# Kernel tuning notes

Hardware: AMD Instinct MI355X
Metric: run time of the kernel (lower is better)

## Reference

```python
import jax, jax.numpy as jnp
import numpy as np

N = 100000   # total nodes
E = 1600000  # total edges
B = 256      # graphs per batch
F_NODE, F_EDGE, H = 35, 10, 64
N_CONV = 3
IN_DIM = 2 * H + F_EDGE  # 138
EPS = 1e-5


def setup_inputs() -> dict:
    key = jax.random.key(0)
    ks = jax.random.split(key, 16)
    node_features = jax.random.normal(ks[0], (N, F_NODE), dtype=jnp.float32)
    edge_index = jax.random.randint(ks[1], (2, E), 0, N, dtype=jnp.int64)
    edge_features = jax.random.uniform(ks[2], (E, F_EDGE), dtype=jnp.float32)
    graph_index = jnp.sort(jax.random.randint(ks[3], (N,), 0, B, dtype=jnp.int64))
    s = lambda fan_in: 1.0 / np.sqrt(fan_in)
    embed_w = jax.random.uniform(ks[4], (F_NODE, H), jnp.float32, -s(F_NODE), s(F_NODE))
    embed_b = jax.random.uniform(ks[5], (H,), jnp.float32, -s(F_NODE), s(F_NODE))
    gate_w = jax.random.uniform(ks[6], (N_CONV, IN_DIM, H), jnp.float32, -s(IN_DIM), s(IN_DIM))
    gate_b = jax.random.uniform(ks[7], (N_CONV, H), jnp.float32, -s(IN_DIM), s(IN_DIM))
    cand_w = jax.random.uniform(ks[8], (N_CONV, IN_DIM, H), jnp.float32, -s(IN_DIM), s(IN_DIM))
    cand_b = jax.random.uniform(ks[9], (N_CONV, H), jnp.float32, -s(IN_DIM), s(IN_DIM))
    bn_g = jnp.ones((N_CONV, H), dtype=jnp.float32)
    bn_b = jnp.zeros((N_CONV, H), dtype=jnp.float32)
    mlp_w1 = jax.random.uniform(ks[10], (H, 128), jnp.float32, -s(H), s(H))
    mlp_b1 = jax.random.uniform(ks[11], (128,), jnp.float32, -s(H), s(H))
    mlp_w2 = jax.random.uniform(ks[12], (128, 64), jnp.float32, -s(128), s(128))
    mlp_b2 = jax.random.uniform(ks[13], (64,), jnp.float32, -s(128), s(128))
    mlp_w3 = jax.random.uniform(ks[14], (64, 1), jnp.float32, -s(64), s(64))
    mlp_b3 = jax.random.uniform(ks[15], (1,), jnp.float32, -s(64), s(64))
    return dict(node_features=node_features, edge_index=edge_index,
                edge_features=edge_features, graph_index=graph_index,
                embed_w=embed_w, embed_b=embed_b,
                gate_w=gate_w, gate_b=gate_b, cand_w=cand_w, cand_b=cand_b,
                bn_g=bn_g, bn_b=bn_b,
                mlp_w1=mlp_w1, mlp_b1=mlp_b1, mlp_w2=mlp_w2, mlp_b2=mlp_b2,
                mlp_w3=mlp_w3, mlp_b3=mlp_b3)


def _conv(h, src, dst, edge_feat, gw, gb, cw, cb, gamma, beta):
    # gather -> concat -> gated message
    z = jnp.concatenate([h[src], h[dst], edge_feat], axis=1)  # [E, 2H+F_edge]
    g = jax.nn.sigmoid(z @ gw + gb)
    c = jax.nn.softplus(z @ cw + cb)
    m = g * c
    # scatter-add onto source nodes
    agg = jax.ops.segment_sum(m, src, num_segments=h.shape[0])
    # BatchNorm1d (training-mode batch stats, biased variance)
    mu = agg.mean(axis=0)
    var = agg.var(axis=0)
    agg_bn = (agg - mu) * jax.lax.rsqrt(var + EPS) * gamma + beta
    return jax.nn.softplus(h + agg_bn)


def reference(node_features, edge_index, edge_features, graph_index,
              embed_w, embed_b, gate_w, gate_b, cand_w, cand_b, bn_g, bn_b,
              mlp_w1, mlp_b1, mlp_w2, mlp_b2, mlp_w3, mlp_b3):
    src, dst = edge_index[0], edge_index[1]
    h = node_features @ embed_w + embed_b  # [N, H]
    for i in range(N_CONV):
        h = _conv(h, src, dst, edge_features,
                  gate_w[i], gate_b[i], cand_w[i], cand_b[i], bn_g[i], bn_b[i])
    # mean pool per graph (B is static = 256)
    pooled = jax.ops.segment_sum(h, graph_index, num_segments=B)
    counts = jax.ops.segment_sum(jnp.ones((h.shape[0],), h.dtype), graph_index, num_segments=B)
    pooled = pooled / jnp.clip(counts, 1.0, None)[:, None]
    x = jax.nn.softplus(pooled @ mlp_w1 + mlp_b1)
    x = jax.nn.softplus(x @ mlp_w2 + mlp_b2)
    return (x @ mlp_w3 + mlp_b3)[:, 0]  # [B]
```

## Files before the change

kernel.cpp:

```cpp
#include <hip/hip_runtime.h>
#include <hip/hip_bf16.h>

#define NN 100000
#define EE 1600000
#define BB 256
#define F_NODE 35
#define F_EDGE 10
#define HH 64
#define IN_DIM 138
#define N_CONV 3
#define EPSBN 1e-5f
#define NB1 ((NN + 255) / 256)

#define NWAVES 2000
#define NGROUPS 50
#define SUBLEN 200
#define EPW 800
#define EFSTR 12

typedef _Float16 half8 __attribute__((ext_vector_type(8)));
typedef float floatx4 __attribute__((ext_vector_type(4)));

__device__ __forceinline__ float softplus_fast(float x) {
    return fmaxf(x, 0.0f) + __logf(1.0f + __expf(-fabsf(x)));
}
__device__ __forceinline__ float sigmoid_fast(float x) {
    return __builtin_amdgcn_rcpf(1.0f + __expf(-x));
}

__global__ __launch_bounds__(256)
void hist_kernel(const int* __restrict__ src, int* __restrict__ cnt) {
    int e = blockIdx.x * 256 + threadIdx.x;
    atomicAdd(&cnt[src[e]], 1);
}

__global__ __launch_bounds__(256)
void scan1_kernel(int* __restrict__ cnt, int* __restrict__ bsum, int n) {
    __shared__ int ls[256];
    int t = threadIdx.x;
    int i = blockIdx.x * 256 + t;
    int v = (i < n) ? cnt[i] : 0;
    ls[t] = v;
    __syncthreads();
#pragma unroll
    for (int off = 1; off < 256; off <<= 1) {
        int add = (t >= off) ? ls[t - off] : 0;
        __syncthreads();
        ls[t] += add;
        __syncthreads();
    }
    if (i < n) cnt[i] = ls[t] - v;
    if (t == 255) bsum[blockIdx.x] = ls[255];
}

__global__ __launch_bounds__(512)
void scan2_kernel(int* __restrict__ bsum, int nb) {
    __shared__ int ls[512];
    int t = threadIdx.x;
    int v = (t < nb) ? bsum[t] : 0;
    ls[t] = v;
    __syncthreads();
#pragma unroll
    for (int off = 1; off < 512; off <<= 1) {
        int add = (t >= off) ? ls[t - off] : 0;
        __syncthreads();
        ls[t] += add;
        __syncthreads();
    }
    if (t < nb) bsum[t] = ls[t] - v;
}

__global__ __launch_bounds__(256)
void scan3_kernel(int* __restrict__ cnt, const int* __restrict__ bsum, int n) {
    int i = blockIdx.x * 256 + threadIdx.x;
    if (i < n) cnt[i] += bsum[blockIdx.x];
}

__global__ __launch_bounds__(256)
void scatter_kernel(const int* __restrict__ src, const int* __restrict__ dst,
                    const float* __restrict__ ef,
                    int* __restrict__ offs,
                    int* __restrict__ ssorted, int* __restrict__ dsorted,
                    _Float16* __restrict__ ef16) {
    int e = blockIdx.x * 256 + threadIdx.x;
    int s = src[e];
    int pos = atomicAdd(&offs[s], 1);
    ssorted[pos] = s;
    dsorted[pos] = dst[e];
    const float* efe = ef + (size_t)e * F_EDGE;
    uint* op = (uint*)(ef16 + (size_t)pos * EFSTR);
#pragma unroll
    for (int i = 0; i < 5; i++) {
        _Float16 h0 = (_Float16)efe[2 * i];
        _Float16 h1 = (_Float16)efe[2 * i + 1];
        op[i] = (uint)*(unsigned short*)&h0 | ((uint)*(unsigned short*)&h1 << 16);
    }
    op[5] = 0u;
}

__global__ __launch_bounds__(256)
void prep_w_kernel(const float* __restrict__ gw, const float* __restrict__ cw,
                   _Float16* __restrict__ wT) {
    int idx = blockIdx.x * 256 + threadIdx.x;
    if (idx >= 3 * 128 * 160) return;
    int k = idx % 160;
    int n = (idx / 160) & 127;
    int layer = idx / (160 * 128);
    float v = 0.f;
    if (k < IN_DIM)
        v = (n < 64) ? gw[layer * IN_DIM * HH + k * HH + n]
                     : cw[layer * IN_DIM * HH + k * HH + (n - 64)];
    wT[idx] = (_Float16)v;
}

__global__ __launch_bounds__(256)
void embed_kernel(const float* __restrict__ nf, const float* __restrict__ w,
                  const float* __restrict__ bias, float* __restrict__ h,
                  _Float16* __restrict__ h16, int n) {
    __shared__ float wl[F_NODE * HH];
    int tid = threadIdx.x;
    for (int i = tid; i < F_NODE * HH; i += 256) wl[i] = w[i];
    __syncthreads();
    int idx = blockIdx.x * 256 + tid;
    int node = idx >> 6, j = idx & 63;
    if (node >= n) return;
    float acc = bias[j];
    const float* row = nf + node * F_NODE;
#pragma unroll
    for (int k = 0; k < F_NODE; k++) acc += row[k] * wl[k * HH + j];
    h[idx] = acc;
    h16[idx] = (_Float16)acc;
}

__device__ __forceinline__ void load_A(const _Float16* __restrict__ h16,
                                       const _Float16* __restrict__ ef16,
                                       int s, int d, int eg, int quad,
                                       uint4& A0, uint4& A1, uint4& A2, uint4& A3,
                                       uint4& A4) {
    const uint4* hs = (const uint4*)(h16 + (size_t)s * HH);
    const uint4* hd = (const uint4*)(h16 + (size_t)d * HH);
    A0 = hs[quad];
    A1 = hs[quad + 4];
    A2 = hd[quad];
    A3 = hd[quad + 4];
    uint4 z; z.x = z.y = z.z = z.w = 0u;
    A4 = z;
    const _Float16* p = ef16 + (size_t)eg * EFSTR;
    if (quad == 0) {
        uint2 a = *(const uint2*)p;
        uint2 b = *(const uint2*)(p + 4);
        A4.x = a.x; A4.y = a.y; A4.z = b.x; A4.w = b.y;
    } else if (quad == 1) {
        uint2 a = *(const uint2*)(p + 8);
        A4.x = a.x; A4.y = a.y;
    }
}

__global__ __launch_bounds__(64, 2)
void edge_conv_mfma(const _Float16* __restrict__ h16,
                    const int* __restrict__ esrc,
                    const int* __restrict__ edst,
                    const _Float16* __restrict__ ef16,
                    const _Float16* __restrict__ wT,
                    const float* __restrict__ gb, const float* __restrict__ cb,
                    float* __restrict__ agg) {
    int lane = threadIdx.x;
    int quad = lane >> 4, n15 = lane & 15;
    int base = blockIdx.x * EPW + ((n15 >> 2) * SUBLEN) + (n15 & 3);

    half8 B[8][5];
#pragma unroll
    for (int t = 0; t < 8; t++) {
        const _Float16* wr = wT + (t * 16 + n15) * 160 + quad * 8;
#pragma unroll
        for (int ks = 0; ks < 5; ks++)
            B[t][ks] = *(const half8*)(wr + ks * 32);
    }
    float gb0 = gb[n15], gb1 = gb[16 + n15], gb2 = gb[32 + n15], gb3 = gb[48 + n15];
    float cb0 = cb[n15], cb1 = cb[16 + n15], cb2 = cb[32 + n15], cb3 = cb[48 + n15];

    int sprev = -1;
    float am0 = 0.f, am1 = 0.f, am2 = 0.f, am3 = 0.f;

    int eg = base;
    int s = esrc[eg], d = edst[eg];
    uint4 A0, A1, A2, A3, A4;
    load_A(h16, ef16, s, d, eg, quad, A0, A1, A2, A3, A4);
    int egn = base + 4;
    int sn = esrc[egn], dn = edst[egn];

    for (int g = 0; g < NGROUPS; g++) {
        int s_cur = s;

        floatx4 acc[8];
#pragma unroll
        for (int t = 0; t < 8; t++) acc[t] = (floatx4){0.f, 0.f, 0.f, 0.f};

        half8 a0 = __builtin_bit_cast(half8, A0);
        half8 a1 = __builtin_bit_cast(half8, A1);
        half8 a2 = __builtin_bit_cast(half8, A2);
        half8 a3 = __builtin_bit_cast(half8, A3);
        half8 a4 = __builtin_bit_cast(half8, A4);
#pragma unroll
        for (int t = 0; t < 8; t++) acc[t] = __builtin_amdgcn_mfma_f32_16x16x32_f16(a0, B[t][0], acc[t], 0, 0, 0);
#pragma unroll
        for (int t = 0; t < 8; t++) acc[t] = __builtin_amdgcn_mfma_f32_16x16x32_f16(a1, B[t][1], acc[t], 0, 0, 0);
#pragma unroll
        for (int t = 0; t < 8; t++) acc[t] = __builtin_amdgcn_mfma_f32_16x16x32_f16(a2, B[t][2], acc[t], 0, 0, 0);
#pragma unroll
        for (int t = 0; t < 8; t++) acc[t] = __builtin_amdgcn_mfma_f32_16x16x32_f16(a3, B[t][3], acc[t], 0, 0, 0);
#pragma unroll
        for (int t = 0; t < 8; t++) acc[t] = __builtin_amdgcn_mfma_f32_16x16x32_f16(a4, B[t][4], acc[t], 0, 0, 0);

        int egc = base + ((g + 1 < NGROUPS) ? (g + 1) * 4 : g * 4);
        load_A(h16, ef16, sn, dn, egc, quad, A0, A1, A2, A3, A4);
        s = sn; d = dn;
        int eg2 = base + ((g + 2 < NGROUPS) ? (g + 2) * 4 : (NGROUPS - 1) * 4);
        sn = esrc[eg2]; dn = edst[eg2];

#pragma unroll
        for (int r = 0; r < 4; r++) {
            int sr = __shfl(s_cur, quad * 4 + r, 64);
            if (sr != sprev) {
                if (sprev >= 0) {
                    float* p = agg + (size_t)sprev * HH + n15;
                    atomicAdd(p, am0);
                    atomicAdd(p + 16, am1);
                    atomicAdd(p + 32, am2);
                    atomicAdd(p + 48, am3);
                }
                sprev = sr;
                am0 = am1 = am2 = am3 = 0.f;
            }
            am0 += sigmoid_fast(acc[0][r] + gb0) * softplus_fast(acc[4][r] + cb0);
            am1 += sigmoid_fast(acc[1][r] + gb1) * softplus_fast(acc[5][r] + cb1);
            am2 += sigmoid_fast(acc[2][r] + gb2) * softplus_fast(acc[6][r] + cb2);
            am3 += sigmoid_fast(acc[3][r] + gb3) * softplus_fast(acc[7][r] + cb3);
        }
    }
    if (sprev >= 0) {
        float* p = agg + (size_t)sprev * HH + n15;
        atomicAdd(p, am0);
        atomicAdd(p + 16, am1);
        atomicAdd(p + 32, am2);
        atomicAdd(p + 48, am3);
    }
}

__global__ __launch_bounds__(256)
void bn_stats_kernel(const float* __restrict__ agg, float* __restrict__ stats, int total) {
    __shared__ float ls[256], lss[256];
    int tid = threadIdx.x;
    float s = 0.f, ss = 0.f;
    for (int idx = blockIdx.x * 256 + tid; idx < total; idx += gridDim.x * 256) {
        float v = agg[idx];
        s += v;
        ss += v * v;
    }
    ls[tid] = s;
    lss[tid] = ss;
    __syncthreads();
    if (tid < 64) {
        s = ls[tid] + ls[tid + 64] + ls[tid + 128] + ls[tid + 192];
        ss = lss[tid] + lss[tid + 64] + lss[tid + 128] + lss[tid + 192];
        atomicAdd(&stats[tid], s);
        atomicAdd(&stats[64 + tid], ss);
    }
}

__global__ __launch_bounds__(256)
void bn_update_kernel(float* __restrict__ h, _Float16* __restrict__ h16,
                      const float* __restrict__ agg,
                      const float* __restrict__ stats,
                      const float* __restrict__ g, const float* __restrict__ b,
                      int total, float invN) {
    int idx = blockIdx.x * 256 + threadIdx.x;
    if (idx >= total) return;
    int j = idx & 63;
    float mu = stats[j] * invN;
    float var = stats[64 + j] * invN - mu * mu;
    var = fmaxf(var, 0.0f);
    float scale = g[j] * rsqrtf(var + EPSBN);
    float v = h[idx] + (agg[idx] - mu) * scale + b[j];
    float hv = softplus_fast(v);
    h[idx] = hv;
    h16[idx] = (_Float16)hv;
}

__global__ __launch_bounds__(256)
void pool_kernel(const float* __restrict__ h, const int* __restrict__ gi,
                 float* __restrict__ pool, float* __restrict__ counts, int n) {
    int tid = threadIdx.x;
    int grp = tid >> 6;
    int j = tid & 63;
    int n0 = blockIdx.x * 64 + grp * 16;
    if (n0 >= n) return;
    int nend = n0 + 16; if (nend > n) nend = n;
    int gprev = gi[n0];
    float a = 0.f;
    int cnt = 0;
    for (int nn = n0; nn < nend; nn++) {
        int gg = gi[nn];
        if (gg != gprev) {
            atomicAdd(&pool[gprev * 64 + j], a);
            if (j == 0) atomicAdd(&counts[gprev], (float)cnt);
            a = 0.f; cnt = 0; gprev = gg;
        }
        a += h[(size_t)nn * 64 + j];
        cnt++;
    }
    atomicAdd(&pool[gprev * 64 + j], a);
    if (j == 0) atomicAdd(&counts[gprev], (float)cnt);
}

__global__ __launch_bounds__(128)
void mlp_kernel(const float* __restrict__ pool, const float* __restrict__ counts,
                const float* __restrict__ w1, const float* __restrict__ b1,
                const float* __restrict__ w2, const float* __restrict__ b2,
                const float* __restrict__ w3, const float* __restrict__ b3,
                float* __restrict__ out) {
    __shared__ float x0[64], x1[128], x2[64];
    int b = blockIdx.x, t = threadIdx.x;
    if (t < 64) {
        float c = counts[b];
        c = c < 1.f ? 1.f : c;
        x0[t] = pool[b * 64 + t] / c;
    }
    __syncthreads();
    {
        float acc = 0.f;
#pragma unroll
        for (int k = 0; k < 64; k++) acc += x0[k] * w1[k * 128 + t];
        x1[t] = softplus_fast(acc + b1[t]);
    }
    __syncthreads();
    if (t < 64) {
        float acc = 0.f;
#pragma unroll
        for (int k = 0; k < 128; k++) acc += x1[k] * w2[k * 64 + t];
        x2[t] = softplus_fast(acc + b2[t]);
    }
    __syncthreads();
    if (t == 0) {
        float acc = 0.f;
        for (int k = 0; k < 64; k++) acc += x2[k] * w3[k];
        out[b] = acc + b3[0];
    }
}

extern "C" void kernel_launch(void* const* d_in, const int* in_sizes, int n_in,
                              void* d_out, int out_size, void* d_ws, size_t ws_size,
                              hipStream_t stream) {
    const float* nf      = (const float*)d_in[0];
    const int*   ei      = (const int*)d_in[1];
    const float* ef      = (const float*)d_in[2];
    const int*   gi      = (const int*)d_in[3];
    const float* embed_w = (const float*)d_in[4];
    const float* embed_b = (const float*)d_in[5];
    const float* gate_w  = (const float*)d_in[6];
    const float* gate_b  = (const float*)d_in[7];
    const float* cand_w  = (const float*)d_in[8];
    const float* cand_b  = (const float*)d_in[9];
    const float* bn_g    = (const float*)d_in[10];
    const float* bn_b    = (const float*)d_in[11];
    const float* w1      = (const float*)d_in[12];
    const float* b1      = (const float*)d_in[13];
    const float* w2      = (const float*)d_in[14];
    const float* b2      = (const float*)d_in[15];
    const float* w3      = (const float*)d_in[16];
    const float* b3      = (const float*)d_in[17];
    float* out = (float*)d_out;

    const int NH = NN * HH;
    char* p = (char*)d_ws;
    float*     h       = (float*)p;            p += (size_t)NH * 4;
    float*     agg     = (float*)p;            p += (size_t)NH * 4;
    float*     stats   = (float*)p;            p += 128 * 4;
    _Float16*  h16     = (_Float16*)p;         p += (size_t)NH * 2;
    int*       ssorted = (int*)p;              p += (size_t)EE * 4;
    int*       dsorted = (int*)p;              p += (size_t)EE * 4;
    _Float16*  ef16    = (_Float16*)p;         p += (size_t)EE * EFSTR * 2;
    _Float16*  wTall   = (_Float16*)p;         p += (size_t)3 * 128 * 160 * 2;
    int*       offs    = (int*)p;              p += (size_t)NN * 4;
    int*       bsum    = (int*)p;              p += 512 * 4;
    float*     pool    = (float*)p;            p += (size_t)BB * HH * 4;
    float*     counts  = (float*)p;            p += (size_t)BB * 4;

    const int* src = ei;
    const int* dst = ei + EE;

    hipMemsetAsync(offs, 0, (size_t)NN * 4, stream);
    hist_kernel<<<EE / 256, 256, 0, stream>>>(src, offs);
    prep_w_kernel<<<(3 * 128 * 160 + 255) / 256, 256, 0, stream>>>(gate_w, cand_w, wTall);
    scan1_kernel<<<NB1, 256, 0, stream>>>(offs, bsum, NN);
    scan2_kernel<<<1, 512, 0, stream>>>(bsum, NB1);
    scan3_kernel<<<NB1, 256, 0, stream>>>(offs, bsum, NN);
    scatter_kernel<<<EE / 256, 256, 0, stream>>>(src, dst, ef, offs, ssorted, dsorted, ef16);

    embed_kernel<<<NH / 256, 256, 0, stream>>>(nf, embed_w, embed_b, h, h16, NN);

    for (int i = 0; i < N_CONV; i++) {
        hipMemsetAsync(agg, 0, ((size_t)NH + 128) * 4, stream);
        edge_conv_mfma<<<NWAVES, 64, 0, stream>>>(
            h16, ssorted, dsorted, ef16,
            wTall + (size_t)i * 128 * 160,
            gate_b + i * HH, cand_b + i * HH, agg);
        bn_stats_kernel<<<512, 256, 0, stream>>>(agg, stats, NH);
        bn_update_kernel<<<NH / 256, 256, 0, stream>>>(
            h, h16, agg, stats, bn_g + i * HH, bn_b + i * HH, NH, 1.0f / (float)NN);
    }

    hipMemsetAsync(pool, 0, (size_t)(BB * HH + BB) * 4, stream);
    pool_kernel<<<(NN + 63) / 64, 256, 0, stream>>>(h, gi, pool, counts, NN);
    mlp_kernel<<<BB, 128, 0, stream>>>(pool, counts, w1, b1, w2, b2, w3, b3, out);
}
```

Before: 969.0 us.

## Build edge sort via rank/perm gather and fold agg zeroing into BN update

Records each edge's rank during the histogram atomics, then builds a permutation and gathers edge data in sorted order. This replaces the scatter kernel's second round of atomics and its scattered writes with coalesced writes and gathered reads, and reads edge features as float2. It also merges all memsets into one at the start, keeps per-layer stats buffers, and has bn_update zero agg after reading it, so the per-layer memsets go away. The cost is an extra kernel launch and two extra E-sized buffers (perm, rank).

New measurement: 895.0 us. -7.6%, faster.

```diff
diff --git a/kernel.cpp b/kernel.cpp
--- a/kernel.cpp
+++ b/kernel.cpp
@@ -29,9 +29,10 @@
 }
 
 __global__ __launch_bounds__(256)
-void hist_kernel(const int* __restrict__ src, int* __restrict__ cnt) {
+void hist_rank_kernel(const int* __restrict__ src, int* __restrict__ cnt,
+                      int* __restrict__ rank) {
     int e = blockIdx.x * 256 + threadIdx.x;
-    atomicAdd(&cnt[src[e]], 1);
+    rank[e] = atomicAdd(&cnt[src[e]], 1);
 }
 
 __global__ __launch_bounds__(256)
@@ -77,22 +78,29 @@
 }
 
 __global__ __launch_bounds__(256)
-void scatter_kernel(const int* __restrict__ src, const int* __restrict__ dst,
-                    const float* __restrict__ ef,
-                    int* __restrict__ offs,
-                    int* __restrict__ ssorted, int* __restrict__ dsorted,
-                    _Float16* __restrict__ ef16) {
+void perm_kernel(const int* __restrict__ src, const int* __restrict__ rank,
+                 const int* __restrict__ offs, int* __restrict__ perm) {
     int e = blockIdx.x * 256 + threadIdx.x;
-    int s = src[e];
-    int pos = atomicAdd(&offs[s], 1);
-    ssorted[pos] = s;
+    perm[offs[src[e]] + rank[e]] = e;
+}
+
+__global__ __launch_bounds__(256)
+void gather_kernel(const int* __restrict__ perm,
+                   const int* __restrict__ src, const int* __restrict__ dst,
+                   const float* __restrict__ ef,
+                   int* __restrict__ ssorted, int* __restrict__ dsorted,
+                   _Float16* __restrict__ ef16) {
+    int pos = blockIdx.x * 256 + threadIdx.x;
+    int e = perm[pos];
+    ssorted[pos] = src[e];
     dsorted[pos] = dst[e];
-    const float* efe = ef + (size_t)e * F_EDGE;
+    const float2* efe = (const float2*)(ef + (size_t)e * F_EDGE);
     uint* op = (uint*)(ef16 + (size_t)pos * EFSTR);
 #pragma unroll
     for (int i = 0; i < 5; i++) {
-        _Float16 h0 = (_Float16)efe[2 * i];
-        _Float16 h1 = (_Float16)efe[2 * i + 1];
+        float2 v = efe[i];
+        _Float16 h0 = (_Float16)v.x;
+        _Float16 h1 = (_Float16)v.y;
         op[i] = (uint)*(unsigned short*)&h0 | ((uint)*(unsigned short*)&h1 << 16);
     }
     op[5] = 0u;
@@ -270,7 +278,7 @@
 
 __global__ __launch_bounds__(256)
 void bn_update_kernel(float* __restrict__ h, _Float16* __restrict__ h16,
-                      const float* __restrict__ agg,
+                      float* __restrict__ agg,
                       const float* __restrict__ stats,
                       const float* __restrict__ g, const float* __restrict__ b,
                       int total, float invN) {
@@ -281,7 +289,9 @@
     float var = stats[64 + j] * invN - mu * mu;
     var = fmaxf(var, 0.0f);
     float scale = g[j] * rsqrtf(var + EPSBN);
-    float v = h[idx] + (agg[idx] - mu) * scale + b[j];
+    float a = agg[idx];
+    agg[idx] = 0.f;
+    float v = h[idx] + (a - mu) * scale + b[j];
     float hv = softplus_fast(v);
     h[idx] = hv;
     h16[idx] = (_Float16)hv;
@@ -373,44 +383,47 @@
 
     const int NH = NN * HH;
     char* p = (char*)d_ws;
+    int*       offs    = (int*)p;              p += (size_t)NN * 4;
+    float*     agg     = (float*)p;            p += (size_t)NH * 4;
+    float*     stats   = (float*)p;            p += 3 * 128 * 4;
+    float*     pool    = (float*)p;            p += (size_t)BB * HH * 4;
+    float*     counts  = (float*)p;            p += (size_t)BB * 4;
+    size_t zero_bytes = (size_t)(p - (char*)d_ws);
     float*     h       = (float*)p;            p += (size_t)NH * 4;
-    float*     agg     = (float*)p;            p += (size_t)NH * 4;
-    float*     stats   = (float*)p;            p += 128 * 4;
     _Float16*  h16     = (_Float16*)p;         p += (size_t)NH * 2;
     int*       ssorted = (int*)p;              p += (size_t)EE * 4;
     int*       dsorted = (int*)p;              p += (size_t)EE * 4;
     _Float16*  ef16    = (_Float16*)p;         p += (size_t)EE * EFSTR * 2;
+    int*       perm    = (int*)p;              p += (size_t)EE * 4;
+    int*       rank    = (int*)p;              p += (size_t)EE * 4;
     _Float16*  wTall   = (_Float16*)p;         p += (size_t)3 * 128 * 160 * 2;
-    int*       offs    = (int*)p;              p += (size_t)NN * 4;
     int*       bsum    = (int*)p;              p += 512 * 4;
-    float*     pool    = (float*)p;            p += (size_t)BB * HH * 4;
-    float*     counts  = (float*)p;            p += (size_t)BB * 4;
 
     const int* src = ei;
     const int* dst = ei + EE;
 
-    hipMemsetAsync(offs, 0, (size_t)NN * 4, stream);
-    hist_kernel<<<EE / 256, 256, 0, stream>>>(src, offs);
+    hipMemsetAsync(d_ws, 0, zero_bytes, stream);
+
+    hist_rank_kernel<<<EE / 256, 256, 0, stream>>>(src, offs, rank);
     prep_w_kernel<<<(3 * 128 * 160 + 255) / 256, 256, 0, stream>>>(gate_w, cand_w, wTall);
     scan1_kernel<<<NB1, 256, 0, stream>>>(offs, bsum, NN);
     scan2_kernel<<<1, 512, 0, stream>>>(bsum, NB1);
     scan3_kernel<<<NB1, 256, 0, stream>>>(offs, bsum, NN);
-    scatter_kernel<<<EE / 256, 256, 0, stream>>>(src, dst, ef, offs, ssorted, dsorted, ef16);
+    perm_kernel<<<EE / 256, 256, 0, stream>>>(src, rank, offs, perm);
+    gather_kernel<<<EE / 256, 256, 0, stream>>>(perm, src, dst, ef, ssorted, dsorted, ef16);
 
     embed_kernel<<<NH / 256, 256, 0, stream>>>(nf, embed_w, embed_b, h, h16, NN);
 
     for (int i = 0; i < N_CONV; i++) {
-        hipMemsetAsync(agg, 0, ((size_t)NH + 128) * 4, stream);
         edge_conv_mfma<<<NWAVES, 64, 0, stream>>>(
             h16, ssorted, dsorted, ef16,
             wTall + (size_t)i * 128 * 160,
             gate_b + i * HH, cand_b + i * HH, agg);
-        bn_stats_kernel<<<512, 256, 0, stream>>>(agg, stats, NH);
+        bn_stats_kernel<<<512, 256, 0, stream>>>(agg, stats + i * 128, NH);
         bn_update_kernel<<<NH / 256, 256, 0, stream>>>(
-            h, h16, agg, stats, bn_g + i * HH, bn_b + i * HH, NH, 1.0f / (float)NN);
-    }
-
-    hipMemsetAsync(pool, 0, (size_t)(BB * HH + BB) * 4, stream);
+            h, h16, agg, stats + i * 128, bn_g + i * HH, bn_b + i * HH, NH, 1.0f / (float)NN);
+    }
+
     pool_kernel<<<(NN + 63) / 64, 256, 0, stream>>>(h, gi, pool, counts, NN);
     mlp_kernel<<<BB, 128, 0, stream>>>(pool, counts, w1, b1, w2, b2, w3, b3, out);
 }
```
